# Performance work log

Hardware: AMD Instinct MI355X
Metric: run time of the kernel (lower is better)

The kernel has to match this reference:

```python
import jax, jax.numpy as jnp
import numpy as np

MAX_SLOTS = 8192


def _compress_lowest_importance_pair(x):
    """Vectorized version of the per-batch python loop: merge the adjacent pair
    with the lowest summed L2-norm into one averaged slot. [B,S,d] -> [B,S-1,d]."""
    B, S, d = x.shape
    imp = jnp.linalg.norm(x, axis=-1)              # [B, S]
    pair_scores = imp[:, :-1] + imp[:, 1:]          # [B, S-1]
    p = jnp.argmin(pair_scores, axis=1)             # [B] merge index per row
    idx = jnp.arange(S - 1)                         # output slot positions
    # gather: out[j] = x[j] for j<=p, x[j+1] for j>p
    g = idx[None, :] + (idx[None, :] > p[:, None]).astype(idx.dtype)  # [B, S-1]
    out = jnp.take_along_axis(x, g[:, :, None], axis=1)               # [B, S-1, d]
    left = jnp.take_along_axis(x, p[:, None, None], axis=1)           # [B, 1, d]
    right = jnp.take_along_axis(x, (p + 1)[:, None, None], axis=1)    # [B, 1, d]
    merged = 0.5 * (left + right)
    # overwrite position p with the merged slot
    out = jnp.where(idx[None, :, None] == p[:, None, None], merged, out)
    return out


def _compress_oldest_pair(x):
    merged = 0.5 * (x[:, :1, :] + x[:, 1:2, :])
    return jnp.concatenate([merged, x[:, 2:, :]], axis=1)


def setup_inputs() -> dict:
    key = jax.random.key(0)
    k1, k2 = jax.random.split(key)
    bank_states = jax.random.normal(k1, (16, 8192, 512), dtype=jnp.float32)
    refresh_states = jax.random.normal(k2, (16, 32, 512), dtype=jnp.float32)
    return {"bank_states": bank_states, "refresh_states": refresh_states}


def reference(bank_states, refresh_states):
    # write(): refresh_states.detach(); sizes here take the concat+compress path
    refresh = jax.lax.stop_gradient(refresh_states)
    updated = jnp.concatenate([bank_states, refresh], axis=1)  # [B, S_bank+S_ref, d]
    # shapes are static, so this python while unrolls a fixed number of steps
    while updated.shape[1] > MAX_SLOTS:
        if updated.shape[1] <= 2:
            updated = _compress_oldest_pair(updated)
        else:
            updated = _compress_lowest_importance_pair(updated)
    return updated
```

## Files before the change

kernel.cpp:

```cpp
#include <hip/hip_runtime.h>
#include <cstdint>
#include <cstddef>

#define B_DIM  16
#define S_BANK 8192
#define S_REF  32
#define S_TOT  8224
#define NMERGE 32
#define D      512
#define NCH    129

typedef float vfloat4 __attribute__((ext_vector_type(4)));
typedef unsigned long long u64;
#define DEADPK 0xFFFFFFFFFFFFFFFFULL

__device__ __forceinline__ int d_lo(double d){ union{double d; int i[2];}u; u.d=d; return u.i[0]; }
__device__ __forceinline__ int d_hi(double d){ union{double d; int i[2];}u; u.d=d; return u.i[1]; }
__device__ __forceinline__ double d_mk(int hi,int lo){ union{double d; int i[2];}u; u.i[0]=lo;u.i[1]=hi; return u.d; }
__device__ __forceinline__ int u_lo(u64 v){ return (int)(v & 0xFFFFFFFFULL); }
__device__ __forceinline__ int u_hi(u64 v){ return (int)(v >> 32); }
__device__ __forceinline__ u64 u_mk(int hi,int lo){ return ((u64)(unsigned)hi << 32) | (u64)(unsigned)lo; }
__device__ __forceinline__ u64 d_bits(double d){ union{double d; u64 u;}x; x.d=d; return x.u; }

__device__ __forceinline__ u64 pack_score(double s, int j) {
    return (d_bits(s) & ~0x3FFFULL) | (u64)(unsigned)j;
}

template<int CTRL, int ROWM>
__device__ __forceinline__ u64 dpp_u64(u64 v) {
    int lo = __builtin_amdgcn_update_dpp(u_lo(v), u_lo(v), CTRL, ROWM, 0xF, false);
    int hi = __builtin_amdgcn_update_dpp(u_hi(v), u_hi(v), CTRL, ROWM, 0xF, false);
    return u_mk(hi, lo);
}
__device__ __forceinline__ u64 rl_u64(u64 v, int l) {
    int lo = __builtin_amdgcn_readlane(u_lo(v), l);
    int hi = __builtin_amdgcn_readlane(u_hi(v), l);
    return u_mk(hi, lo);
}
__device__ __forceinline__ u64 lexmin_wave_u64(u64 v) {
    u64 w;
    w = dpp_u64<0x111,0xF>(v); if (w < v) v = w;
    w = dpp_u64<0x112,0xF>(v); if (w < v) v = w;
    w = dpp_u64<0x114,0xF>(v); if (w < v) v = w;
    w = dpp_u64<0x118,0xF>(v); if (w < v) v = w;
    w = dpp_u64<0x142,0xF>(v); if (w < v) v = w;
    w = dpp_u64<0x143,0xF>(v); if (w < v) v = w;
    return rl_u64(v, 63);
}
__device__ __forceinline__ u64 scan_min_incl(u64 v) {
    u64 w;
    w = dpp_u64<0x111,0xF>(v); if (w < v) v = w;
    w = dpp_u64<0x112,0xF>(v); if (w < v) v = w;
    w = dpp_u64<0x114,0xF>(v); if (w < v) v = w;
    w = dpp_u64<0x118,0xF>(v); if (w < v) v = w;
    w = dpp_u64<0x142,0xA>(v); if (w < v) v = w;
    w = dpp_u64<0x143,0xC>(v); if (w < v) v = w;
    return v;
}
__device__ __forceinline__ u64 scan_min_suffix(u64 v, int lane) {
    u64 w;
    w = dpp_u64<0x101,0xF>(v); if (w < v) v = w;
    w = dpp_u64<0x102,0xF>(v); if (w < v) v = w;
    w = dpp_u64<0x104,0xF>(v); if (w < v) v = w;
    w = dpp_u64<0x108,0xF>(v); if (w < v) v = w;
    u64 t16 = rl_u64(v, 16), t32 = rl_u64(v, 32), t48 = rl_u64(v, 48);
    u64 s3 = t48;
    u64 s2 = (t32 < s3) ? t32 : s3;
    u64 s1 = (t16 < s2) ? t16 : s2;
    int row = lane >> 4;
    u64 add = (row == 0) ? s1 : (row == 1) ? s2 : (row == 2) ? s3 : DEADPK;
    if (add < v) v = add;
    return v;
}
template<int CTRL>
__device__ __forceinline__ void sum_level(double& v) {
    int lo2 = __builtin_amdgcn_update_dpp(0, d_lo(v), CTRL, 0xF, 0xF, true);
    int hi2 = __builtin_amdgcn_update_dpp(0, d_hi(v), CTRL, 0xF, 0xF, true);
    v += d_mk(hi2, lo2);
}
__device__ __forceinline__ double sum_wave(double v) {
    sum_level<0x111>(v); sum_level<0x112>(v); sum_level<0x114>(v);
    sum_level<0x118>(v); sum_level<0x142>(v); sum_level<0x143>(v);
    int lo = __builtin_amdgcn_readlane(d_lo(v), 63);
    int hi = __builtin_amdgcn_readlane(d_hi(v), 63);
    return d_mk(hi, lo);
}

__global__ __launch_bounds__(256) void norms_kernel(const float* __restrict__ bank,
                                                    const float* __restrict__ refresh,
                                                    double* __restrict__ norms) {
    int gw_lin = (int)((blockIdx.x * 256 + threadIdx.x) >> 6);
    int gw   = B_DIM * S_TOT - 1 - gw_lin;
    int lane = threadIdx.x & 63;
    int b = gw / S_TOT;
    int s = gw - b * S_TOT;
    const float4* src = (const float4*)(s < S_BANK
        ? bank    + ((size_t)b * S_BANK + s) * D
        : refresh + ((size_t)b * S_REF + (s - S_BANK)) * D);
    float4 f0 = src[lane];
    float4 f1 = src[lane + 64];
    double acc = 0.0;
    acc += (double)f0.x * f0.x + (double)f0.y * f0.y + (double)f0.z * f0.z + (double)f0.w * f0.w;
    acc += (double)f1.x * f1.x + (double)f1.y * f1.y + (double)f1.z * f1.z + (double)f1.w * f1.w;
    acc = sum_wave(acc);
    if (lane == 0) norms[gw] = sqrt(acc);
}

__global__ __launch_bounds__(256) void chunkmin_kernel(const double* __restrict__ norms,
                                                       u64* __restrict__ c_pk_g) {
    int w    = (int)((blockIdx.x * 256 + threadIdx.x) >> 6);
    int lane = threadIdx.x & 63;
    if (w >= B_DIM * NCH) return;
    int b = w / NCH;
    int c = w - b * NCH;
    int j = c * 64 + lane;
    u64 pk = DEADPK;
    if (j <= S_TOT - 2) {
        double a = norms[b * S_TOT + j];
        double d = norms[b * S_TOT + j + 1];
        pk = pack_score(a + d, j);
    }
    pk = lexmin_wave_u64(pk);
    if (lane == 0) c_pk_g[b * NCH + c] = pk;
}

__device__ __forceinline__ const float* slot_gptr(int id, int b,
        const float* bank, const float* refresh) {
    return (id < S_BANK) ? bank    + ((size_t)b * S_BANK + id) * D
                         : refresh + ((size_t)b * S_REF + (id - S_BANK)) * D;
}

struct FastLds {
    u64   pref[192];
    u64   suf[192];
    float stage[34][D];
    int   s_pred[34];
    int   s_map[80];
};
struct FallLds {
    unsigned short s_next[S_TOT];
    float          s_mvec[NMERGE][D];
    unsigned short s_mpos[NMERGE];
    unsigned short s_dead[NMERGE];
};
union MergeLds { FastLds fast; FallLds fall; };

__global__ __launch_bounds__(256) void merge_kernel(const float* __restrict__ bank,
        const float* __restrict__ refresh, const double* __restrict__ norms,
        const u64* __restrict__ c_pk_g,
        float* __restrict__ merged, unsigned short* __restrict__ idx_out) {
    __shared__ double  s_imp[S_TOT];
    __shared__ u64     c_pk[NCH];
    __shared__ MergeLds u;
    __shared__ int     rec_L[NMERGE], rec_R[NMERGE];
    __shared__ u64     rec_chosen[NMERGE];
    __shared__ u64     s_PL, s_SR;
    __shared__ int     s_flag;

    const int t    = threadIdx.x;
    const int b    = blockIdx.x;
    const int lane = t & 63;
    const int wid  = t >> 6;
    const double INF = __builtin_inf();

    if (t < NCH) c_pk[t] = c_pk_g[b * NCH + t];
    __syncthreads();

    u64 pk_min0;
    {
        u64 a = c_pk[lane];
        u64 bq = c_pk[lane + 64];
        u64 c = (lane == 0) ? c_pk[128] : DEADPK;
        u64 m = (a < bq) ? a : bq;
        m = (m < c) ? m : c;
        pk_min0 = lexmin_wave_u64(m);
    }
    const int p0 = (int)(pk_min0 & 0x3FFFULL);

    const int cmid = p0 >> 6;
    int wsx = cmid - 1;
    if (wsx < 0) wsx = 0;
    if (wsx > NCH - 3) wsx = NCH - 3;
    const int ws  = wsx;
    const int wlo = ws * 64;

    int do_fall = 1;
    {
        FastLds& F = u.fast;
        int mb = p0 - 40;
        if (mb < 0) mb = 0;
        if (mb > S_TOT - 80) mb = S_TOT - 80;
        const int mbase = mb;

        for (int j = t; j < 194; j += 256) {
            int g = wlo + j;
            if (g < S_TOT) s_imp[g] = norms[b * S_TOT + g];
        }
        for (int j = t; j < 80; j += 256) F.s_map[j] = -1;
        __syncthreads();

        if (t == 0) {
            int Lp = p0, Rp = p0 + 1;
            F.s_pred[0] = p0;     F.s_map[p0 - mbase] = 0;
            F.s_pred[1] = p0 + 1; F.s_map[p0 + 1 - mbase] = 1;
            for (int i = 2; i < 34; ++i) {
                double dl = (Lp >= 1)         ? s_imp[Lp - 1] : INF;
                double dr = (Rp + 1 < S_TOT)  ? s_imp[Rp + 1] : INF;
                bool goL = !(dr < dl);
                int pos = goL ? (Lp - 1) : (Rp + 1);
                if (goL) --Lp; else ++Rp;
                F.s_pred[i] = pos; F.s_map[pos - mbase] = i;
            }
        }
        __syncthreads();

        for (int s = wid; s < 34; s += 4) {
            int pos = F.s_pred[s];
            const float4* g = (const float4*)slot_gptr(pos, b, bank, refresh);
            float4 v0 = g[2 * lane], v1 = g[2 * lane + 1];
            float4* dstg = (float4*)&F.stage[s][0];
            dstg[2 * lane] = v0; dstg[2 * lane + 1] = v1;
        }
        __syncthreads();

        float4 m0r, m1r;
        double nrm;
        int L = p0, R = p0 + 1;
        {
            const float4* ga = (const float4*)&F.stage[0][0];
            const float4* gb = (const float4*)&F.stage[1][0];
            float4 a0 = ga[2 * lane], a1 = ga[2 * lane + 1];
            float4 b0 = gb[2 * lane], b1 = gb[2 * lane + 1];
            m0r.x = 0.5f * (a0.x + b0.x); m0r.y = 0.5f * (a0.y + b0.y);
            m0r.z = 0.5f * (a0.z + b0.z); m0r.w = 0.5f * (a0.w + b0.w);
            m1r.x = 0.5f * (a1.x + b1.x); m1r.y = 0.5f * (a1.y + b1.y);
            m1r.z = 0.5f * (a1.z + b1.z); m1r.w = 0.5f * (a1.w + b1.w);
            double ss = 0.0;
            ss += (double)m0r.x * m0r.x + (double)m0r.y * m0r.y + (double)m0r.z * m0r.z + (double)m0r.w * m0r.w;
            ss += (double)m1r.x * m1r.x + (double)m1r.y * m1r.y + (double)m1r.z * m1r.z + (double)m1r.w * m1r.w;
            nrm = sqrt(sum_wave(ss));
            if (t == 0) { rec_L[0] = L; rec_R[0] = R; rec_chosen[0] = pk_min0; }
        }
        for (int step = 1; step < NMERGE; ++step) {
            const int cl = L - 1, cr = R + 1;
            const bool hasL = (cl >= 0);
            const bool hasR = (cr < S_TOT);
            float4 xl0 = {0,0,0,0}, xl1 = {0,0,0,0}, xr0 = {0,0,0,0}, xr1 = {0,0,0,0};
            double il = INF, ir = INF;
            if (hasL) {
                il = s_imp[cl];
                const int rlm = F.s_map[cl - mbase];
                if (rlm >= 0) { const float4* g = (const float4*)&F.stage[rlm][0];
                                xl0 = g[2 * lane]; xl1 = g[2 * lane + 1]; }
                else          { const float4* g = (const float4*)slot_gptr(cl, b, bank, refresh);
                                xl0 = g[2 * lane]; xl1 = g[2 * lane + 1]; }
            }
            if (hasR) {
                ir = s_imp[cr];
                const int rrm = F.s_map[cr - mbase];
                if (rrm >= 0) { const float4* g = (const float4*)&F.stage[rrm][0];
                                xr0 = g[2 * lane]; xr1 = g[2 * lane + 1]; }
                else          { const float4* g = (const float4*)slot_gptr(cr, b, bank, refresh);
                                xr0 = g[2 * lane]; xr1 = g[2 * lane + 1]; }
            }
            const u64 pkL = hasL ? pack_score(il + nrm, cl) : DEADPK;
            const u64 pkR = hasR ? pack_score(nrm + ir, L)  : DEADPK;
            const bool goL = (pkL < pkR);
            const u64 chosen = goL ? pkL : pkR;
            float4 a0, a1, b0, b1;
            if (goL) { a0 = xl0; a1 = xl1; b0 = m0r; b1 = m1r; L = cl; }
            else     { a0 = m0r; a1 = m1r; b0 = xr0; b1 = xr1; R = cr; }
            m0r.x = 0.5f * (a0.x + b0.x); m0r.y = 0.5f * (a0.y + b0.y);
            m0r.z = 0.5f * (a0.z + b0.z); m0r.w = 0.5f * (a0.w + b0.w);
            m1r.x = 0.5f * (a1.x + b1.x); m1r.y = 0.5f * (a1.y + b1.y);
            m1r.z = 0.5f * (a1.z + b1.z); m1r.w = 0.5f * (a1.w + b1.w);
            double ss = 0.0;
            ss += (double)m0r.x * m0r.x + (double)m0r.y * m0r.y + (double)m0r.z * m0r.z + (double)m0r.w * m0r.w;
            ss += (double)m1r.x * m1r.x + (double)m1r.y * m1r.y + (double)m1r.z * m1r.z + (double)m1r.w * m1r.w;
            nrm = sqrt(sum_wave(ss));
            if (t == 0) { rec_L[step] = L; rec_R[step] = R; rec_chosen[step] = chosen; }
        }
        __syncthreads();

        if (wid < 3) {
            int c = ws + wid;
            int idx = c * 64 + lane;
            u64 pk0 = (idx <= S_TOT - 2) ? pack_score(s_imp[idx] + s_imp[idx + 1], idx)
                                         : DEADPK;
            F.pref[idx - wlo] = scan_min_incl(pk0);
            F.suf[idx - wlo]  = scan_min_suffix(pk0, lane);
        }
        if (wid == 3) {
            u64 x0 = (lane < ws) ? c_pk[lane] : DEADPK;
            u64 x1 = (lane + 64 < ws) ? c_pk[lane + 64] : DEADPK;
            u64 pl = (x0 < x1) ? x0 : x1;
            pl = lexmin_wave_u64(pl);
            u64 y0 = (lane > ws + 2) ? c_pk[lane] : DEADPK;
            u64 y1 = (lane + 64 > ws + 2) ? c_pk[lane + 64] : DEADPK;
            u64 y2 = (lane == 0 && 128 > ws + 2) ? c_pk[128] : DEADPK;
            u64 sr = (y0 < y1) ? y0 : y1;
            sr = (sr < y2) ? sr : y2;
            sr = lexmin_wave_u64(sr);
            if (lane == 0) { s_PL = pl; s_SR = sr; }
        }
        __syncthreads();

        if (wid == 0) {
            u64 cf0 = F.pref[63], cf1 = F.pref[127];
            u64 sf1 = F.suf[64],  sf2 = F.suf[128];
            u64 PL = s_PL, SR = s_SR;
            bool ok = true;
            if (lane >= 1 && lane < NMERGE) {
                int Lp = rec_L[lane - 1], Rp = rec_R[lane - 1];
                int q1 = Lp - 2 - wlo;
                u64 ol = DEADPK;
                if (q1 >= 0) {
                    ol = F.pref[q1];
                    int r1 = q1 >> 6;
                    if (r1 >= 1 && cf0 < ol) ol = cf0;
                    if (r1 >= 2 && cf1 < ol) ol = cf1;
                }
                if (PL < ol) ol = PL;
                int q2 = Rp + 1 - wlo;
                u64 orr = F.suf[q2];
                int r2 = q2 >> 6;
                if (r2 <= 0 && sf1 < orr) orr = sf1;
                if (r2 <= 1 && sf2 < orr) orr = sf2;
                if (SR < orr) orr = SR;
                u64 O = (ol < orr) ? ol : orr;
                ok = rec_chosen[lane] < O;
            }
            if (lane == 0) ok = ok && (rec_R[NMERGE - 1] - rec_L[NMERGE - 1] == NMERGE);
            unsigned long long bad = __ballot(!ok);
            if (lane == 0) s_flag = (bad != 0ULL) ? 1 : 0;
        }
        __syncthreads();

        if (s_flag == 0) {
            if (wid == 0) {
                float4* dst = (float4*)(merged + ((size_t)b * NMERGE + (NMERGE - 1)) * D);
                dst[2 * lane] = m0r; dst[2 * lane + 1] = m1r;
            }
            const int Ls = rec_L[NMERGE - 1], Rs = rec_R[NMERGE - 1];
            for (int j = t; j < S_TOT; j += 256) {
                if (j < Ls)       idx_out[b * S_BANK + j] = (unsigned short)j;
                else if (j == Ls) idx_out[b * S_BANK + j] = (unsigned short)(S_TOT + NMERGE - 1);
                else if (j > Rs)  idx_out[b * S_BANK + j - NMERGE] = (unsigned short)j;
            }
            do_fall = 0;
        }
    }

    if (do_fall) {
        FallLds& G = u.fall;
        for (int j = t; j < S_TOT; j += 256)
            s_imp[j] = norms[b * S_TOT + j];
        for (int j = t; j < S_TOT; j += 256)
            G.s_next[j] = (unsigned short)((j + 1 < S_TOT) ? (j + 1) : 0xFFFF);
        __syncthreads();

        if (wid == 0) {
            u64 cv0 = c_pk[lane];
            u64 cv1 = c_pk[lane + 64];
            u64 cv2 = (lane == 0) ? c_pk[128] : DEADPK;

            int mpos_reg = -1;
            int prev_p = -1, prev_pv = -1, prev_nk = -1;
            int pvok = 0, nkok = 0;
            float4 mm0, mm1, pva0, pva1, pnk0, pnk1;

            for (int step = 0; step < NMERGE; ++step) {
                u64 m = (cv0 < cv1) ? cv0 : cv1;
                m = (m < cv2) ? m : cv2;
                m = lexmin_wave_u64(m);
                const int p = (int)(m & 0x3FFFULL);

                const bool hitA = pvok && (p == prev_pv);
                const bool hitB = nkok && (p == prev_p);

                int k, nk;
                float4 a0, a1, b0, b1;
                if (hitA) {
                    k = prev_p; nk = prev_nk;
                    a0 = pva0; a1 = pva1; b0 = mm0; b1 = mm1;
                } else if (hitB) {
                    k = prev_nk; nk = G.s_next[k];
                    a0 = mm0; a1 = mm1; b0 = pnk0; b1 = pnk1;
                } else {
                    k = G.s_next[p]; nk = G.s_next[k];
                    unsigned long long bA = __ballot((lane < step) && (mpos_reg == p));
                    const int ia = bA ? (S_TOT + 63 - __clzll(bA)) : p;
                    unsigned long long bB = __ballot((lane < step) && (mpos_reg == k));
                    const int ib = bB ? (S_TOT + 63 - __clzll(bB)) : k;
                    if (ia < S_TOT) { const float4* g = (const float4*)slot_gptr(ia, b, bank, refresh);
                                      a0 = g[2 * lane]; a1 = g[2 * lane + 1]; }
                    else            { const float4* g = (const float4*)&G.s_mvec[ia - S_TOT][0];
                                      a0 = g[2 * lane]; a1 = g[2 * lane + 1]; }
                    if (ib < S_TOT) { const float4* g = (const float4*)slot_gptr(ib, b, bank, refresh);
                                      b0 = g[2 * lane]; b1 = g[2 * lane + 1]; }
                    else            { const float4* g = (const float4*)&G.s_mvec[ib - S_TOT][0];
                                      b0 = g[2 * lane]; b1 = g[2 * lane + 1]; }
                }

                int pv;
                if (hitB) {
                    pv = prev_pv;
                } else {
                    int jq = p - 1 - lane;
                    bool plive = (jq >= 0) && (s_imp[jq] < 1e300);
                    unsigned long long pb = __ballot(plive);
                    pv = pb ? (p - __ffsll((unsigned long long)pb)) : -1;
                }

                const double imp_nk = s_imp[(nk != 0xFFFF) ? nk : 0];
                const double imp_pv = s_imp[(pv >= 0) ? pv : 0];
                const int chp = p >> 6, chk = k >> 6;
                const int chv = (pv >= 0) ? (pv >> 6) : -1;
                const int csB = (chk != chp) ? chk : -1;
                const int csC = (chv >= 0 && chv != chp && chv != chk) ? chv : -1;
                const int jjA = chp * 64 + lane;
                const bool validA = (jjA < S_TOT) && (jjA != k);
                const int rawNxtA = validA ? (int)G.s_next[jjA] : 0xFFFF;
                const double impA = validA ? s_imp[jjA] : INF;
                const int nxtA = (jjA == p) ? nk : rawNxtA;
                const double impNxtA = (nxtA != 0xFFFF) ? s_imp[nxtA] : INF;

                float4 m0, m1;
                m0.x = 0.5f * (a0.x + b0.x); m0.y = 0.5f * (a0.y + b0.y);
                m0.z = 0.5f * (a0.z + b0.z); m0.w = 0.5f * (a0.w + b0.w);
                m1.x = 0.5f * (a1.x + b1.x); m1.y = 0.5f * (a1.y + b1.y);
                m1.z = 0.5f * (a1.z + b1.z); m1.w = 0.5f * (a1.w + b1.w);
                {
                    float4* dst = (float4*)&G.s_mvec[step][0];
                    dst[2 * lane] = m0; dst[2 * lane + 1] = m1;
                }
                if (lane == step) mpos_reg = p;

                if (step + 1 < NMERGE) {
                    prev_p = p; prev_pv = pv; prev_nk = nk;
                    mm0 = m0; mm1 = m1;
                    pvok = (pv >= 0); nkok = (nk != 0xFFFF);
                    unsigned long long bpv = __ballot((lane <= step) && (mpos_reg == pv));
                    const int ipv = bpv ? (S_TOT + 63 - __clzll(bpv)) : pv;
                    unsigned long long bnk = __ballot((lane <= step) && (mpos_reg == nk));
                    const int ink = bnk ? (S_TOT + 63 - __clzll(bnk)) : nk;
                    if (pvok) {
                        if (ipv < S_TOT) { const float4* g = (const float4*)slot_gptr(ipv, b, bank, refresh);
                                           pva0 = g[2 * lane]; pva1 = g[2 * lane + 1]; }
                        else             { const float4* g = (const float4*)&G.s_mvec[ipv - S_TOT][0];
                                           pva0 = g[2 * lane]; pva1 = g[2 * lane + 1]; }
                    }
                    if (nkok) {
                        if (ink < S_TOT) { const float4* g = (const float4*)slot_gptr(ink, b, bank, refresh);
                                           pnk0 = g[2 * lane]; pnk1 = g[2 * lane + 1]; }
                        else             { const float4* g = (const float4*)&G.s_mvec[ink - S_TOT][0];
                                           pnk0 = g[2 * lane]; pnk1 = g[2 * lane + 1]; }
                    }
                }

                double ss = 0.0;
                ss += (double)m0.x * m0.x + (double)m0.y * m0.y + (double)m0.z * m0.z + (double)m0.w * m0.w;
                ss += (double)m1.x * m1.x + (double)m1.y * m1.y + (double)m1.z * m1.z + (double)m1.w * m1.w;
                const double nrm = sqrt(sum_wave(ss));

                if (lane == 0) {
                    G.s_next[p]    = (unsigned short)nk;
                    s_imp[k]       = INF;
                    s_imp[p]       = nrm;
                    G.s_mpos[step] = (unsigned short)p;
                    G.s_dead[step] = (unsigned short)k;
                }

                {
                    u64 sc = DEADPK;
                    if (validA && nxtA != 0xFFFF) {
                        double a0d = (jjA == p) ? nrm : impA;
                        if (a0d < 1e300) {
                            double a1d = (nxtA == p) ? nrm : impNxtA;
                            sc = pack_score(a0d + a1d, jjA);
                        }
                    }
                    sc = lexmin_wave_u64(sc);
                    if (chp < 64)       { if (lane == chp)      cv0 = sc; }
                    else if (chp < 128) { if (lane == chp - 64) cv1 = sc; }
                    else                { if (lane == 0)        cv2 = sc; }
                }
                if (csB >= 0) {
                    int jj = csB * 64 + lane;
                    u64 sc = DEADPK;
                    if (jj < S_TOT && jj != k) {
                        int nxt = (int)G.s_next[jj];
                        if (nxt != 0xFFFF) {
                            double a0d = s_imp[jj];
                            if (a0d < 1e300) sc = pack_score(a0d + s_imp[nxt], jj);
                        }
                    }
                    sc = lexmin_wave_u64(sc);
                    if (csB < 64)       { if (lane == csB)      cv0 = sc; }
                    else if (csB < 128) { if (lane == csB - 64) cv1 = sc; }
                    else                { if (lane == 0)        cv2 = sc; }
                }
                if (csC >= 0) {
                    int jj = csC * 64 + lane;
                    u64 sc = DEADPK;
                    if (jj < S_TOT && jj != k) {
                        int nxt = (int)G.s_next[jj];
                        if (nxt != 0xFFFF) {
                            double a0d = s_imp[jj];
                            if (a0d < 1e300) sc = pack_score(a0d + s_imp[nxt], jj);
                        }
                    }
                    sc = lexmin_wave_u64(sc);
                    if (csC < 64)       { if (lane == csC)      cv0 = sc; }
                    else if (csC < 128) { if (lane == csC - 64) cv1 = sc; }
                    else                { if (lane == 0)        cv2 = sc; }
                }
            }
        }
        __syncthreads();

        {
            const float4* src = (const float4*)&G.s_mvec[0][0];
            float4* dst = (float4*)(merged + (size_t)b * NMERGE * D);
            for (int i = t; i < NMERGE * D / 4; i += 256) dst[i] = src[i];
        }
        for (int j = t; j < S_TOT; j += 256) G.s_next[j] = 0xFFFF;
        __syncthreads();
        if (t == 0)
            for (int m2 = 0; m2 < NMERGE; ++m2) G.s_next[G.s_mpos[m2]] = (unsigned short)m2;
        __syncthreads();
        for (int j = t; j < S_TOT; j += 256) {
            if (s_imp[j] < 1e300) {
                int r = j;
                #pragma unroll
                for (int m2 = 0; m2 < NMERGE; ++m2) r -= (G.s_dead[m2] < j) ? 1 : 0;
                unsigned short lut = G.s_next[j];
                idx_out[b * S_BANK + r] = (lut != 0xFFFF) ? (unsigned short)(S_TOT + lut)
                                                          : (unsigned short)j;
            }
        }
    }
}

__global__ __launch_bounds__(256) void gather_kernel(const vfloat4* __restrict__ bank,
        const vfloat4* __restrict__ refresh, const vfloat4* __restrict__ merged,
        const unsigned short* __restrict__ idx, vfloat4* __restrict__ out) {
    size_t tid = (size_t)blockIdx.x * 256 + threadIdx.x;
    int slot = (int)(tid >> 7);
    int c    = (int)(tid & 127);
    int b    = slot >> 13;
    int src  = idx[slot];
    const vfloat4* sp;
    if (src < S_BANK)     sp = bank    + ((size_t)b * S_BANK + src) * (D / 4);
    else if (src < S_TOT) sp = refresh + ((size_t)b * S_REF + (src - S_BANK)) * (D / 4);
    else                  sp = merged  + ((size_t)b * NMERGE + (src - S_TOT)) * (D / 4);
    vfloat4 v = sp[c];
    __builtin_nontemporal_store(v, &out[tid]);
}

extern "C" void kernel_launch(void* const* d_in, const int* in_sizes, int n_in,
                              void* d_out, int out_size, void* d_ws, size_t ws_size,
                              hipStream_t stream) {
    const float* bank    = (const float*)d_in[0];
    const float* refresh = (const float*)d_in[1];

    double*         norms  = (double*)d_ws;
    float*          merged = (float*)((char*)d_ws + (size_t)B_DIM * S_TOT * sizeof(double));
    unsigned short* idx    = (unsigned short*)((char*)merged + (size_t)B_DIM * NMERGE * D * sizeof(float));
    u64*            c_pk_g = (u64*)((char*)idx + (size_t)B_DIM * S_BANK * sizeof(unsigned short));
    float*          out    = (float*)d_out;

    norms_kernel<<<(B_DIM * S_TOT) / 4, 256, 0, stream>>>(bank, refresh, norms);
    chunkmin_kernel<<<(B_DIM * NCH * 64 + 255) / 256, 256, 0, stream>>>(norms, c_pk_g);
    merge_kernel<<<B_DIM, 256, 0, stream>>>(bank, refresh, norms, c_pk_g, merged, idx);
    gather_kernel<<<(size_t)B_DIM * S_BANK * (D / 4) / 256, 256, 0, stream>>>(
        (const vfloat4*)bank, (const vfloat4*)refresh, (const vfloat4*)merged, idx, (vfloat4*)out);
}
```

Measured before the change: 149.2 us.

## Replace LDS staging with register prefetch and overlap merge chain with prefix scans

```diff
diff --git a/kernel.cpp b/kernel.cpp
--- a/kernel.cpp
+++ b/kernel.cpp
@@ -131,11 +131,8 @@
 }
 
 struct FastLds {
-    u64   pref[192];
-    u64   suf[192];
-    float stage[34][D];
-    int   s_pred[34];
-    int   s_map[80];
+    u64 pref[192];
+    u64 suf[192];
 };
 struct FallLds {
     unsigned short s_next[S_TOT];
@@ -184,53 +181,37 @@
     const int ws  = wsx;
     const int wlo = ws * 64;
 
+    float4 m0r, m1r;
+
     int do_fall = 1;
     {
         FastLds& F = u.fast;
-        int mb = p0 - 40;
-        if (mb < 0) mb = 0;
-        if (mb > S_TOT - 80) mb = S_TOT - 80;
-        const int mbase = mb;
 
         for (int j = t; j < 194; j += 256) {
             int g = wlo + j;
             if (g < S_TOT) s_imp[g] = norms[b * S_TOT + g];
         }
-        for (int j = t; j < 80; j += 256) F.s_map[j] = -1;
-        __syncthreads();
-
-        if (t == 0) {
-            int Lp = p0, Rp = p0 + 1;
-            F.s_pred[0] = p0;     F.s_map[p0 - mbase] = 0;
-            F.s_pred[1] = p0 + 1; F.s_map[p0 + 1 - mbase] = 1;
-            for (int i = 2; i < 34; ++i) {
-                double dl = (Lp >= 1)         ? s_imp[Lp - 1] : INF;
-                double dr = (Rp + 1 < S_TOT)  ? s_imp[Rp + 1] : INF;
-                bool goL = !(dr < dl);
-                int pos = goL ? (Lp - 1) : (Rp + 1);
-                if (goL) --Lp; else ++Rp;
-                F.s_pred[i] = pos; F.s_map[pos - mbase] = i;
-            }
-        }
-        __syncthreads();
-
-        for (int s = wid; s < 34; s += 4) {
-            int pos = F.s_pred[s];
-            const float4* g = (const float4*)slot_gptr(pos, b, bank, refresh);
-            float4 v0 = g[2 * lane], v1 = g[2 * lane + 1];
-            float4* dstg = (float4*)&F.stage[s][0];
-            dstg[2 * lane] = v0; dstg[2 * lane + 1] = v1;
-        }
-        __syncthreads();
-
-        float4 m0r, m1r;
-        double nrm;
-        int L = p0, R = p0 + 1;
-        {
-            const float4* ga = (const float4*)&F.stage[0][0];
-            const float4* gb = (const float4*)&F.stage[1][0];
-            float4 a0 = ga[2 * lane], a1 = ga[2 * lane + 1];
-            float4 b0 = gb[2 * lane], b1 = gb[2 * lane + 1];
+        __syncthreads();
+
+        if (wid == 0) {
+            const float4* gA = (const float4*)slot_gptr(p0, b, bank, refresh);
+            const float4* gB = (const float4*)slot_gptr(p0 + 1, b, bank, refresh);
+            float4 a0 = gA[2 * lane], a1 = gA[2 * lane + 1];
+            float4 b0 = gB[2 * lane], b1 = gB[2 * lane + 1];
+            int q;
+            q = (p0 - 1 >= 0) ? p0 - 1 : 0;
+            const float4* gq = (const float4*)slot_gptr(q, b, bank, refresh);
+            float4 cL0 = gq[2 * lane], cL1 = gq[2 * lane + 1];
+            q = (p0 + 2 <= S_TOT - 1) ? p0 + 2 : S_TOT - 1;
+            gq = (const float4*)slot_gptr(q, b, bank, refresh);
+            float4 cR0 = gq[2 * lane], cR1 = gq[2 * lane + 1];
+            q = (p0 - 2 >= 0) ? p0 - 2 : 0;
+            gq = (const float4*)slot_gptr(q, b, bank, refresh);
+            float4 fL0 = gq[2 * lane], fL1 = gq[2 * lane + 1];
+            q = (p0 + 3 <= S_TOT - 1) ? p0 + 3 : S_TOT - 1;
+            gq = (const float4*)slot_gptr(q, b, bank, refresh);
+            float4 fR0 = gq[2 * lane], fR1 = gq[2 * lane + 1];
+
             m0r.x = 0.5f * (a0.x + b0.x); m0r.y = 0.5f * (a0.y + b0.y);
             m0r.z = 0.5f * (a0.z + b0.z); m0r.w = 0.5f * (a0.w + b0.w);
             m1r.x = 0.5f * (a1.x + b1.x); m1r.y = 0.5f * (a1.y + b1.y);
@@ -238,70 +219,69 @@
             double ss = 0.0;
             ss += (double)m0r.x * m0r.x + (double)m0r.y * m0r.y + (double)m0r.z * m0r.z + (double)m0r.w * m0r.w;
             ss += (double)m1r.x * m1r.x + (double)m1r.y * m1r.y + (double)m1r.z * m1r.z + (double)m1r.w * m1r.w;
-            nrm = sqrt(sum_wave(ss));
+            double nrm = sqrt(sum_wave(ss));
+            int L = p0, R = p0 + 1;
             if (t == 0) { rec_L[0] = L; rec_R[0] = R; rec_chosen[0] = pk_min0; }
-        }
-        for (int step = 1; step < NMERGE; ++step) {
-            const int cl = L - 1, cr = R + 1;
-            const bool hasL = (cl >= 0);
-            const bool hasR = (cr < S_TOT);
-            float4 xl0 = {0,0,0,0}, xl1 = {0,0,0,0}, xr0 = {0,0,0,0}, xr1 = {0,0,0,0};
-            double il = INF, ir = INF;
-            if (hasL) {
-                il = s_imp[cl];
-                const int rlm = F.s_map[cl - mbase];
-                if (rlm >= 0) { const float4* g = (const float4*)&F.stage[rlm][0];
-                                xl0 = g[2 * lane]; xl1 = g[2 * lane + 1]; }
-                else          { const float4* g = (const float4*)slot_gptr(cl, b, bank, refresh);
-                                xl0 = g[2 * lane]; xl1 = g[2 * lane + 1]; }
-            }
-            if (hasR) {
-                ir = s_imp[cr];
-                const int rrm = F.s_map[cr - mbase];
-                if (rrm >= 0) { const float4* g = (const float4*)&F.stage[rrm][0];
-                                xr0 = g[2 * lane]; xr1 = g[2 * lane + 1]; }
-                else          { const float4* g = (const float4*)slot_gptr(cr, b, bank, refresh);
-                                xr0 = g[2 * lane]; xr1 = g[2 * lane + 1]; }
-            }
-            const u64 pkL = hasL ? pack_score(il + nrm, cl) : DEADPK;
-            const u64 pkR = hasR ? pack_score(nrm + ir, L)  : DEADPK;
-            const bool goL = (pkL < pkR);
-            const u64 chosen = goL ? pkL : pkR;
-            float4 a0, a1, b0, b1;
-            if (goL) { a0 = xl0; a1 = xl1; b0 = m0r; b1 = m1r; L = cl; }
-            else     { a0 = m0r; a1 = m1r; b0 = xr0; b1 = xr1; R = cr; }
-            m0r.x = 0.5f * (a0.x + b0.x); m0r.y = 0.5f * (a0.y + b0.y);
-            m0r.z = 0.5f * (a0.z + b0.z); m0r.w = 0.5f * (a0.w + b0.w);
-            m1r.x = 0.5f * (a1.x + b1.x); m1r.y = 0.5f * (a1.y + b1.y);
-            m1r.z = 0.5f * (a1.z + b1.z); m1r.w = 0.5f * (a1.w + b1.w);
-            double ss = 0.0;
-            ss += (double)m0r.x * m0r.x + (double)m0r.y * m0r.y + (double)m0r.z * m0r.z + (double)m0r.w * m0r.w;
-            ss += (double)m1r.x * m1r.x + (double)m1r.y * m1r.y + (double)m1r.z * m1r.z + (double)m1r.w * m1r.w;
-            nrm = sqrt(sum_wave(ss));
-            if (t == 0) { rec_L[step] = L; rec_R[step] = R; rec_chosen[step] = chosen; }
-        }
-        __syncthreads();
-
-        if (wid < 3) {
-            int c = ws + wid;
+
+            for (int step = 1; step < NMERGE; ++step) {
+                const int cl = L - 1, cr = R + 1;
+                const bool hasL = (cl >= 0);
+                const bool hasR = (cr < S_TOT);
+                const double il = hasL ? s_imp[cl] : INF;
+                const double ir = hasR ? s_imp[cr] : INF;
+                const u64 pkL = hasL ? pack_score(il + nrm, cl) : DEADPK;
+                const u64 pkR = hasR ? pack_score(nrm + ir, L)  : DEADPK;
+                const bool goL = (pkL < pkR);
+                const u64 chosen = goL ? pkL : pkR;
+                float4 a0s, a1s, b0s, b1s;
+                if (goL) { a0s = cL0; a1s = cL1; b0s = m0r; b1s = m1r; }
+                else     { a0s = m0r; a1s = m1r; b0s = cR0; b1s = cR1; }
+                m0r.x = 0.5f * (a0s.x + b0s.x); m0r.y = 0.5f * (a0s.y + b0s.y);
+                m0r.z = 0.5f * (a0s.z + b0s.z); m0r.w = 0.5f * (a0s.w + b0s.w);
+                m1r.x = 0.5f * (a1s.x + b1s.x); m1r.y = 0.5f * (a1s.y + b1s.y);
+                m1r.z = 0.5f * (a1s.z + b1s.z); m1r.w = 0.5f * (a1s.w + b1s.w);
+                if (goL) {
+                    L = cl;
+                    cL0 = fL0; cL1 = fL1;
+                    int nq = (L - 2 >= 0) ? L - 2 : 0;
+                    const float4* gp = (const float4*)slot_gptr(nq, b, bank, refresh);
+                    fL0 = gp[2 * lane]; fL1 = gp[2 * lane + 1];
+                } else {
+                    R = cr;
+                    cR0 = fR0; cR1 = fR1;
+                    int nq = (R + 2 <= S_TOT - 1) ? R + 2 : S_TOT - 1;
+                    const float4* gp = (const float4*)slot_gptr(nq, b, bank, refresh);
+                    fR0 = gp[2 * lane]; fR1 = gp[2 * lane + 1];
+                }
+                double ss2 = 0.0;
+                ss2 += (double)m0r.x * m0r.x + (double)m0r.y * m0r.y + (double)m0r.z * m0r.z + (double)m0r.w * m0r.w;
+                ss2 += (double)m1r.x * m1r.x + (double)m1r.y * m1r.y + (double)m1r.z * m1r.z + (double)m1r.w * m1r.w;
+                nrm = sqrt(sum_wave(ss2));
+                if (t == 0) { rec_L[step] = L; rec_R[step] = R; rec_chosen[step] = chosen; }
+            }
+        } else {
+            int c = ws + (wid - 1);
             int idx = c * 64 + lane;
             u64 pk0 = (idx <= S_TOT - 2) ? pack_score(s_imp[idx] + s_imp[idx + 1], idx)
                                          : DEADPK;
             F.pref[idx - wlo] = scan_min_incl(pk0);
             F.suf[idx - wlo]  = scan_min_suffix(pk0, lane);
-        }
-        if (wid == 3) {
-            u64 x0 = (lane < ws) ? c_pk[lane] : DEADPK;
-            u64 x1 = (lane + 64 < ws) ? c_pk[lane + 64] : DEADPK;
-            u64 pl = (x0 < x1) ? x0 : x1;
-            pl = lexmin_wave_u64(pl);
-            u64 y0 = (lane > ws + 2) ? c_pk[lane] : DEADPK;
-            u64 y1 = (lane + 64 > ws + 2) ? c_pk[lane + 64] : DEADPK;
-            u64 y2 = (lane == 0 && 128 > ws + 2) ? c_pk[128] : DEADPK;
-            u64 sr = (y0 < y1) ? y0 : y1;
-            sr = (sr < y2) ? sr : y2;
-            sr = lexmin_wave_u64(sr);
-            if (lane == 0) { s_PL = pl; s_SR = sr; }
+            if (wid == 1) {
+                u64 x0 = (lane < ws) ? c_pk[lane] : DEADPK;
+                u64 x1 = (lane + 64 < ws) ? c_pk[lane + 64] : DEADPK;
+                u64 pl = (x0 < x1) ? x0 : x1;
+                pl = lexmin_wave_u64(pl);
+                if (lane == 0) s_PL = pl;
+            }
+            if (wid == 2) {
+                u64 y0 = (lane > ws + 2) ? c_pk[lane] : DEADPK;
+                u64 y1 = (lane + 64 > ws + 2) ? c_pk[lane + 64] : DEADPK;
+                u64 y2 = (lane == 0 && 128 > ws + 2) ? c_pk[128] : DEADPK;
+                u64 sr = (y0 < y1) ? y0 : y1;
+                sr = (sr < y2) ? sr : y2;
+                sr = lexmin_wave_u64(sr);
+                if (lane == 0) s_SR = sr;
+            }
         }
         __syncthreads();
 
```

New measurement: 144.9 us. 1.03x faster.
